# Optimization experiments

Hardware: AMD Instinct MI355X
Metric: run time of the kernel (lower is better)

The kernel has to match this reference:

```python
import jax, jax.numpy as jnp
import numpy as np

STRIDE = 1  # conv stride from __init__


def setup_inputs() -> dict:
    key = jax.random.key(0)
    k1, k2, k3 = jax.random.split(key, 3)
    prot1 = jax.random.normal(k1, (4, 1024, 8, 64), dtype=jnp.float32)
    prot2 = jax.random.normal(k2, (4, 1024, 8, 64), dtype=jnp.float32)
    # W: (no_filters, no_channels, no_dims, window_size)
    W = jax.random.normal(k3, (32, 8, 64, 7), dtype=jnp.float32)
    return {"prot1": prot1, "prot2": prot2, "W": W}


def _project(x, W, stride):
    """Fused equivalent of unfold + broadcast-mul + sum over (C, window).

    x: (N, H, C, D), W: (F, C, D, w) -> (N, F, H', D) with H' = (H - w)//stride + 1.
    This is a grouped 1D conv: D groups, each mixing C input channels into F outputs.
    """
    N, H, C, D = x.shape
    Fn, _, _, w = W.shape
    xg = jnp.transpose(x, (0, 3, 2, 1)).reshape(N, D * C, H)        # (N, D*C, H)
    Wg = jnp.transpose(W, (2, 0, 1, 3)).reshape(D * Fn, C, w)       # (D*F, C, w)
    out = jax.lax.conv_general_dilated(
        xg, Wg, window_strides=(stride,), padding='VALID',
        dimension_numbers=('NCH', 'OIH', 'NCH'), feature_group_count=D)
    Hp = out.shape[-1]
    return jnp.transpose(out.reshape(N, D, Fn, Hp), (0, 2, 3, 1))   # (N, F, H', D)


def reference(prot1, prot2, W):
    q1 = _project(prot1, W, STRIDE)   # (N, F, H1', D)
    q2 = _project(prot2, W, STRIDE)   # (N, F, H2', D)
    H1p, H2p = q1.shape[2], q2.shape[2]
    scale = jnp.sqrt(jnp.asarray(H1p * H2p, dtype=q1.dtype))
    att = jnp.einsum('nfhd,nfgd->nfhg', q1, q2) / scale             # (N, F, H1', H2')
    a = jax.nn.softmax(att, axis=3)
    p1 = jnp.einsum('nfhg,nfgd->nfhd', a, q2)                       # (N, F, H1', D)
    # NB: source does transpose(att, 2, 2) (a no-op) and multiplies the SAME
    # softmax matrix by the UPDATED p1folds; we reproduce that faithfully.
    p2 = jnp.einsum('nfhg,nfgd->nfhd', a, p1)                       # (N, F, H1', D)
    out1 = jnp.tanh(jnp.transpose(p1, (0, 2, 1, 3)))                # (N, H1', F, D)
    out2 = jnp.tanh(jnp.transpose(p2, (0, 2, 1, 3)))
    # Dropout is identity in eval mode (and dropout_p=0.0 here).
    return (out1, out2)
```

## Files before the change

### kernel.cpp

```cpp
#include <hip/hip_runtime.h>
#include <math.h>

typedef __bf16 bf16_t;
typedef bf16_t bf16x4 __attribute__((ext_vector_type(4)));
typedef bf16_t bf16x8 __attribute__((ext_vector_type(8)));
typedef float  f32x16 __attribute__((ext_vector_type(16)));

#define HH 1024
#define CC 8
#define DD 64
#define FF 32
#define WW 7
#define HP 1018
#define HPAD 1024
#define NF 128
#define QOUT (NF*HP*DD)
#define QWS ((size_t)NF*HPAD*DD)

__global__ __launch_bounds__(256) void conv_kernel(
    const float* __restrict__ x1, const float* __restrict__ x2,
    const float* __restrict__ Wt, bf16_t* __restrict__ q1, bf16_t* __restrict__ q2)
{
    const float* x = blockIdx.z ? x2 : x1;
    bf16_t* q = blockIdx.z ? q2 : q1;
    const int nf = blockIdx.y;
    const int n = nf >> 5, f = nf & 31;
    const int tid = threadIdx.x;
    const int d = tid & 63;
    const int strip = tid >> 6;
    const int h0 = blockIdx.x * 32 + strip * 8;

    float w[CC][WW];
#pragma unroll
    for (int c = 0; c < CC; ++c)
#pragma unroll
        for (int j = 0; j < WW; ++j)
            w[c][j] = Wt[((f*CC + c)*DD + d)*WW + j];

    float acc[8];
#pragma unroll
    for (int i = 0; i < 8; ++i) acc[i] = 0.f;

#pragma unroll
    for (int rr = 0; rr < 14; ++rr) {
        const int row = h0 + rr;
        float xr[CC];
        if (row < HH) {
#pragma unroll
            for (int c = 0; c < CC; ++c)
                xr[c] = x[((size_t)(n*HH + row)*CC + c)*DD + d];
        } else {
#pragma unroll
            for (int c = 0; c < CC; ++c) xr[c] = 0.f;
        }
#pragma unroll
        for (int j = 0; j < WW; ++j) {
            const int i = rr - j;
            if (i >= 0 && i < 8) {
#pragma unroll
                for (int c = 0; c < CC; ++c)
                    acc[i] = fmaf(xr[c], w[c][j], acc[i]);
            }
        }
    }
#pragma unroll
    for (int i = 0; i < 8; ++i) {
        const int h = h0 + i;
        const float v = (h < HP) ? acc[i] : 0.f;
        q[((size_t)nf*HPAD + h)*DD + d] = (bf16_t)v;
    }
}

__device__ __forceinline__ float fast_tanh(float x) {
    const float t = __expf(2.f * x);
    return (t - 1.f) / (t + 1.f);
}

template<int MODE>
__global__ __launch_bounds__(256, 2) void flash(
    const bf16_t* __restrict__ q1, const bf16_t* __restrict__ q2,
    const bf16_t* __restrict__ vsrc, bf16_t* __restrict__ p1out,
    float* __restrict__ out)
{
    __shared__ bf16_t As[64*68];
    __shared__ bf16_t Vt[64*68];

    const int head = blockIdx.y;
    const int n = head >> 5, f = head & 31;
    const int tid = threadIdx.x;
    const int w = tid >> 6;
    const int lane = tid & 63;
    const int lid = lane & 31;
    const int half = lane >> 5;
    const int hb = blockIdx.x * 256 + w * 64;

    const size_t qoff = (size_t)head * HPAD * DD;
    const float SCALE = 1.f / 1018.f;

    bf16x8 bq1[2][4];
#pragma unroll
    for (int nt = 0; nt < 2; ++nt)
#pragma unroll
        for (int kt = 0; kt < 4; ++kt)
            bq1[nt][kt] = *(const bf16x8*)&q1[qoff + (size_t)(hb + 32*nt + lid)*DD + 16*kt + 8*half];

    f32x16 O[2][2] = {};
    float lacc[2] = {0.f, 0.f};

    for (int g0 = 0; g0 < HPAD; g0 += 64) {
        __syncthreads();
        {
            const int gq = tid >> 4;
            const int dq = tid & 15;
            bf16x4 r[4];
#pragma unroll
            for (int i = 0; i < 4; ++i) {
                r[i] = *(const bf16x4*)&q2[qoff + (size_t)(g0 + 4*gq + i)*DD + 4*dq];
                *(bf16x4*)&As[(4*gq + i)*68 + 4*dq] = r[i];
            }
            if (MODE == 1) {
#pragma unroll
                for (int i = 0; i < 4; ++i)
                    r[i] = *(const bf16x4*)&vsrc[qoff + (size_t)(g0 + 4*gq + i)*DD + 4*dq];
            }
#pragma unroll
            for (int j = 0; j < 4; ++j) {
                bf16x4 c = { r[0][j], r[1][j], r[2][j], r[3][j] };
                *(bf16x4*)&Vt[(4*dq + j)*68 + 4*gq] = c;
            }
        }
        __syncthreads();

        const bool tail = (g0 + 64 > HP);

#pragma unroll
        for (int mt = 0; mt < 2; ++mt) {
            f32x16 C[2] = {};
#pragma unroll
            for (int kt = 0; kt < 4; ++kt) {
                const int ab = (32*mt + lid)*68 + 16*kt + 8*half;
                bf16x4 a0 = *(const bf16x4*)&As[ab];
                bf16x4 a1 = *(const bf16x4*)&As[ab + 4];
                bf16x8 a = {a0[0],a0[1],a0[2],a0[3],a1[0],a1[1],a1[2],a1[3]};
                C[0] = __builtin_amdgcn_mfma_f32_32x32x16_bf16(a, bq1[0][kt], C[0], 0,0,0);
                C[1] = __builtin_amdgcn_mfma_f32_32x32x16_bf16(a, bq1[1][kt], C[1], 0,0,0);
            }
            bf16x8 af[2][2];
#pragma unroll
            for (int nt = 0; nt < 2; ++nt) {
                float ls = 0.f;
#pragma unroll
                for (int s = 0; s < 16; ++s) {
                    float e = __expf(C[nt][s] * SCALE);
                    if (tail) {
                        const int gg = g0 + 32*mt + (s&3) + 8*(s>>2) + 4*half;
                        if (gg >= HP) e = 0.f;
                    }
                    ls += e;
                    af[nt][s>>3][s&7] = (bf16_t)e;
                }
                lacc[nt] += ls;
            }
#pragma unroll
            for (int u = 0; u < 2; ++u) {
#pragma unroll
                for (int dt = 0; dt < 2; ++dt) {
                    const int vb = (32*dt + lid)*68 + 32*mt + 16*u + 4*half;
                    bf16x4 b0 = *(const bf16x4*)&Vt[vb];
                    bf16x4 b1 = *(const bf16x4*)&Vt[vb + 8];
                    bf16x8 b = {b0[0],b0[1],b0[2],b0[3],b1[0],b1[1],b1[2],b1[3]};
                    O[0][dt] = __builtin_amdgcn_mfma_f32_32x32x16_bf16(af[0][u], b, O[0][dt], 0,0,0);
                    O[1][dt] = __builtin_amdgcn_mfma_f32_32x32x16_bf16(af[1][u], b, O[1][dt], 0,0,0);
                }
            }
        }
    }

    float linv[2];
#pragma unroll
    for (int nt = 0; nt < 2; ++nt) {
        const float l = lacc[nt] + __shfl_xor(lacc[nt], 32);
        linv[nt] = 1.f / l;
    }
#pragma unroll
    for (int ht = 0; ht < 2; ++ht) {
#pragma unroll
        for (int s = 0; s < 16; ++s) {
            const int R = (s&3) + 8*(s>>2) + 4*half;
            const float li = __shfl(linv[ht], R);
            const int hg = hb + 32*ht + R;
            if (hg < HP) {
#pragma unroll
                for (int dt = 0; dt < 2; ++dt) {
                    const int d = 32*dt + lid;
                    const float val = O[ht][dt][s] * li;
                    out[(((size_t)n*HP + hg)*FF + f)*DD + d] = fast_tanh(val);
                    if (MODE == 0)
                        p1out[qoff + (size_t)hg*DD + d] = (bf16_t)val;
                }
            }
        }
    }
}

extern "C" void kernel_launch(void* const* d_in, const int* in_sizes, int n_in,
                              void* d_out, int out_size, void* d_ws, size_t ws_size,
                              hipStream_t stream)
{
    const float* prot1 = (const float*)d_in[0];
    const float* prot2 = (const float*)d_in[1];
    const float* Wt    = (const float*)d_in[2];
    float* out = (float*)d_out;

    bf16_t* q1b = (bf16_t*)d_ws;
    bf16_t* q2b = q1b + QWS;
    bf16_t* p1b = q2b + QWS;

    conv_kernel<<<dim3(32, NF, 2), 256, 0, stream>>>(prot1, prot2, Wt, q1b, q2b);
    flash<0><<<dim3(4, NF), 256, 0, stream>>>(q1b, q2b, q2b, p1b, out);
    flash<1><<<dim3(4, NF), 256, 0, stream>>>(q1b, q2b, p1b, p1b, out + QOUT);
}
```

Before: 233.3 us.

## Stage conv inputs in LDS, prefetch flash tiles, vectorize LDS reads

The conv kernel now has one block per (batch, 32-row chunk) instead of one per filter. Each block stages 38 input rows in shared memory and reuses them across all 32 filters, using a weight tensor that a new prep kernel relays out so loads are coalesced. The flash kernel prefetches the next q2/V tile into registers while the current one is computed. It also stores V transposed with a permuted column order so MFMA operands come from single 16-byte LDS reads, and it switches to a native exp2. The conv grid shrinks to 256 large blocks using about 77KB of LDS each, which limits occupancy and latency hiding.

```diff
diff --git a/kernel.cpp b/kernel.cpp
--- a/kernel.cpp
+++ b/kernel.cpp
@@ -16,58 +16,86 @@
 #define NF 128
 #define QOUT (NF*HP*DD)
 #define QWS ((size_t)NF*HPAD*DD)
+#define LSTR 72
+
+#if __has_builtin(__builtin_amdgcn_exp2f)
+#define EXP2(x) __builtin_amdgcn_exp2f(x)
+#else
+#define EXP2(x) __expf((x) * 0.6931471805599453f)
+#endif
+
+__global__ __launch_bounds__(256) void wprep_kernel(
+    const float* __restrict__ Wt, float* __restrict__ Wp)
+{
+    const int idx = blockIdx.x * 256 + threadIdx.x;
+    if (idx < FF*CC*DD*WW) {
+        const int j = idx % WW;
+        int t = idx / WW;
+        const int d = t % DD; t /= DD;
+        const int c = t % CC;
+        const int f = t / CC;
+        Wp[((f*CC + c)*WW + j)*DD + d] = Wt[idx];
+    }
+}
 
 __global__ __launch_bounds__(256) void conv_kernel(
     const float* __restrict__ x1, const float* __restrict__ x2,
-    const float* __restrict__ Wt, bf16_t* __restrict__ q1, bf16_t* __restrict__ q2)
-{
+    const float* __restrict__ Wp, bf16_t* __restrict__ q1, bf16_t* __restrict__ q2)
+{
+    __shared__ float xs[38*512];
     const float* x = blockIdx.z ? x2 : x1;
     bf16_t* q = blockIdx.z ? q2 : q1;
-    const int nf = blockIdx.y;
-    const int n = nf >> 5, f = nf & 31;
+    const int n = blockIdx.y;
+    const int hb = blockIdx.x * 32;
     const int tid = threadIdx.x;
+
+    const float4* xg = (const float4*)(x + (size_t)n*HH*512);
+    for (int i = tid; i < 38*128; i += 256) {
+        const int row = hb + (i >> 7);
+        float4 v = {0.f, 0.f, 0.f, 0.f};
+        if (row < HH) v = xg[(size_t)row*128 + (i & 127)];
+        *(float4*)&xs[(size_t)i*4] = v;
+    }
+    __syncthreads();
+
     const int d = tid & 63;
-    const int strip = tid >> 6;
-    const int h0 = blockIdx.x * 32 + strip * 8;
-
-    float w[CC][WW];
-#pragma unroll
-    for (int c = 0; c < CC; ++c)
-#pragma unroll
-        for (int j = 0; j < WW; ++j)
-            w[c][j] = Wt[((f*CC + c)*DD + d)*WW + j];
-
-    float acc[8];
-#pragma unroll
-    for (int i = 0; i < 8; ++i) acc[i] = 0.f;
-
-#pragma unroll
-    for (int rr = 0; rr < 14; ++rr) {
-        const int row = h0 + rr;
-        float xr[CC];
-        if (row < HH) {
-#pragma unroll
-            for (int c = 0; c < CC; ++c)
-                xr[c] = x[((size_t)(n*HH + row)*CC + c)*DD + d];
-        } else {
-#pragma unroll
-            for (int c = 0; c < CC; ++c) xr[c] = 0.f;
-        }
-#pragma unroll
-        for (int j = 0; j < WW; ++j) {
-            const int i = rr - j;
-            if (i >= 0 && i < 8) {
+    const int fq = tid >> 6;
+    for (int fi = 0; fi < 8; ++fi) {
+        const int f = fq*8 + fi;
+        float w[CC][WW];
+#pragma unroll
+        for (int c = 0; c < CC; ++c)
+#pragma unroll
+            for (int j = 0; j < WW; ++j)
+                w[c][j] = Wp[((f*CC + c)*WW + j)*DD + d];
+#pragma unroll
+        for (int hc = 0; hc < 2; ++hc) {
+            float acc[16];
+#pragma unroll
+            for (int i = 0; i < 16; ++i) acc[i] = 0.f;
+#pragma unroll
+            for (int rr = 0; rr < 22; ++rr) {
+                float xv[CC];
 #pragma unroll
                 for (int c = 0; c < CC; ++c)
-                    acc[i] = fmaf(xr[c], w[c][j], acc[i]);
-            }
-        }
-    }
-#pragma unroll
-    for (int i = 0; i < 8; ++i) {
-        const int h = h0 + i;
-        const float v = (h < HP) ? acc[i] : 0.f;
-        q[((size_t)nf*HPAD + h)*DD + d] = (bf16_t)v;
+                    xv[c] = xs[(hc*16 + rr)*512 + c*64 + d];
+#pragma unroll
+                for (int j = 0; j < WW; ++j) {
+                    const int i = rr - j;
+                    if (i >= 0 && i < 16) {
+#pragma unroll
+                        for (int c = 0; c < CC; ++c)
+                            acc[i] = fmaf(xv[c], w[c][j], acc[i]);
+                    }
+                }
+            }
+#pragma unroll
+            for (int i = 0; i < 16; ++i) {
+                const int h = hb + hc*16 + i;
+                const float v = (h < HP) ? acc[i] : 0.f;
+                q[((size_t)(n*FF + f)*HPAD + h)*DD + d] = (bf16_t)v;
+            }
+        }
     }
 }
 
@@ -82,8 +110,8 @@
     const bf16_t* __restrict__ vsrc, bf16_t* __restrict__ p1out,
     float* __restrict__ out)
 {
-    __shared__ bf16_t As[64*68];
-    __shared__ bf16_t Vt[64*68];
+    __shared__ __align__(16) bf16_t As[64*LSTR];
+    __shared__ __align__(16) bf16_t Vt[64*LSTR];
 
     const int head = blockIdx.y;
     const int n = head >> 5, f = head & 31;
@@ -95,7 +123,11 @@
     const int hb = blockIdx.x * 256 + w * 64;
 
     const size_t qoff = (size_t)head * HPAD * DD;
-    const float SCALE = 1.f / 1018.f;
+    const float SC = 1.442695041f / 1018.f;
+
+    const int gq = tid >> 4;
+    const int dq = tid & 15;
+    const int cgb = 4*((gq>>1)&1) + 8*(gq&1) + 16*(gq>>2);
 
     bf16x8 bq1[2][4];
 #pragma unroll
@@ -107,29 +139,38 @@
     f32x16 O[2][2] = {};
     float lacc[2] = {0.f, 0.f};
 
+    bf16x4 rA[4], rV[4];
+#pragma unroll
+    for (int i = 0; i < 4; ++i) {
+        rA[i] = *(const bf16x4*)&q2[qoff + (size_t)(4*gq + i)*DD + 4*dq];
+        if (MODE == 1)
+            rV[i] = *(const bf16x4*)&vsrc[qoff + (size_t)(4*gq + i)*DD + 4*dq];
+    }
+
     for (int g0 = 0; g0 < HPAD; g0 += 64) {
         __syncthreads();
+#pragma unroll
+        for (int i = 0; i < 4; ++i)
+            *(bf16x4*)&As[(4*gq + i)*LSTR + 4*dq] = rA[i];
         {
-            const int gq = tid >> 4;
-            const int dq = tid & 15;
-            bf16x4 r[4];
+            const bf16x4* rv = (MODE == 1) ? rV : rA;
+#pragma unroll
+            for (int j = 0; j < 4; ++j) {
+                bf16x4 c = { rv[0][j], rv[1][j], rv[2][j], rv[3][j] };
+                *(bf16x4*)&Vt[(4*dq + j)*LSTR + cgb] = c;
+            }
+        }
+        __syncthreads();
+
+        if (g0 + 64 < HPAD) {
+            const int gn = g0 + 64;
 #pragma unroll
             for (int i = 0; i < 4; ++i) {
-                r[i] = *(const bf16x4*)&q2[qoff + (size_t)(g0 + 4*gq + i)*DD + 4*dq];
-                *(bf16x4*)&As[(4*gq + i)*68 + 4*dq] = r[i];
-            }
-            if (MODE == 1) {
-#pragma unroll
-                for (int i = 0; i < 4; ++i)
-                    r[i] = *(const bf16x4*)&vsrc[qoff + (size_t)(g0 + 4*gq + i)*DD + 4*dq];
-            }
-#pragma unroll
-            for (int j = 0; j < 4; ++j) {
-                bf16x4 c = { r[0][j], r[1][j], r[2][j], r[3][j] };
-                *(bf16x4*)&Vt[(4*dq + j)*68 + 4*gq] = c;
-            }
-        }
-        __syncthreads();
+                rA[i] = *(const bf16x4*)&q2[qoff + (size_t)(gn + 4*gq + i)*DD + 4*dq];
+                if (MODE == 1)
+                    rV[i] = *(const bf16x4*)&vsrc[qoff + (size_t)(gn + 4*gq + i)*DD + 4*dq];
+            }
+        }
 
         const bool tail = (g0 + 64 > HP);
 
@@ -138,10 +179,7 @@
             f32x16 C[2] = {};
 #pragma unroll
             for (int kt = 0; kt < 4; ++kt) {
-                const int ab = (32*mt + lid)*68 + 16*kt + 8*half;
-                bf16x4 a0 = *(const bf16x4*)&As[ab];
-                bf16x4 a1 = *(const bf16x4*)&As[ab + 4];
-                bf16x8 a = {a0[0],a0[1],a0[2],a0[3],a1[0],a1[1],a1[2],a1[3]};
+                bf16x8 a = *(const bf16x8*)&As[(32*mt + lid)*LSTR + 16*kt + 8*half];
                 C[0] = __builtin_amdgcn_mfma_f32_32x32x16_bf16(a, bq1[0][kt], C[0], 0,0,0);
                 C[1] = __builtin_amdgcn_mfma_f32_32x32x16_bf16(a, bq1[1][kt], C[1], 0,0,0);
             }
@@ -151,7 +189,7 @@
                 float ls = 0.f;
 #pragma unroll
                 for (int s = 0; s < 16; ++s) {
-                    float e = __expf(C[nt][s] * SCALE);
+                    float e = EXP2(C[nt][s] * SC);
                     if (tail) {
                         const int gg = g0 + 32*mt + (s&3) + 8*(s>>2) + 4*half;
                         if (gg >= HP) e = 0.f;
@@ -165,10 +203,7 @@
             for (int u = 0; u < 2; ++u) {
 #pragma unroll
                 for (int dt = 0; dt < 2; ++dt) {
-                    const int vb = (32*dt + lid)*68 + 32*mt + 16*u + 4*half;
-                    bf16x4 b0 = *(const bf16x4*)&Vt[vb];
-                    bf16x4 b1 = *(const bf16x4*)&Vt[vb + 8];
-                    bf16x8 b = {b0[0],b0[1],b0[2],b0[3],b1[0],b1[1],b1[2],b1[3]};
+                    bf16x8 b = *(const bf16x8*)&Vt[(32*dt + lid)*LSTR + 32*mt + 16*u + 8*half];
                     O[0][dt] = __builtin_amdgcn_mfma_f32_32x32x16_bf16(af[0][u], b, O[0][dt], 0,0,0);
                     O[1][dt] = __builtin_amdgcn_mfma_f32_32x32x16_bf16(af[1][u], b, O[1][dt], 0,0,0);
                 }
@@ -215,8 +250,10 @@
     bf16_t* q1b = (bf16_t*)d_ws;
     bf16_t* q2b = q1b + QWS;
     bf16_t* p1b = q2b + QWS;
-
-    conv_kernel<<<dim3(32, NF, 2), 256, 0, stream>>>(prot1, prot2, Wt, q1b, q2b);
+    float* Wp   = (float*)(p1b + QWS);
+
+    wprep_kernel<<<dim3(448), 256, 0, stream>>>(Wt, Wp);
+    conv_kernel<<<dim3(32, 4, 2), 256, 0, stream>>>(prot1, prot2, Wp, q1b, q2b);
     flash<0><<<dim3(4, NF), 256, 0, stream>>>(q1b, q2b, q2b, p1b, out);
     flash<1><<<dim3(4, NF), 256, 0, stream>>>(q1b, q2b, p1b, p1b, out + QOUT);
 }
```

Result: faster. 224.5 us (-3.8%).
